# Kernel optimization log

Measured on AMD Instinct MI355X. Metric: run time of the kernel, lower is better.

The kernel has to match this reference:

```python
import jax, jax.numpy as jnp
import numpy as np

N = 50000       # nodes
E = 800000      # edges (avg degree 16)
C_IN = 128
C_OUT = 64
C_HID = 2 * C_OUT  # 128, per Dir_Encoder_GCN


def gcn_conv(x, W, b, src, dst, ew, n):
    """PyG GCNConv: add self-loops (weight 1), symmetric normalization,
    aggregate transformed source features at destination, add bias."""
    loops = jnp.arange(n)
    s = jnp.concatenate([src, loops])                       # [E+N]
    d = jnp.concatenate([dst, loops])                       # [E+N]
    w = jnp.concatenate([ew, jnp.ones((n,), ew.dtype)])     # [E+N]
    deg = jax.ops.segment_sum(w, d, num_segments=n)         # weighted in-degree
    dinv = jnp.where(deg > 0, jax.lax.rsqrt(deg), 0.0)      # deg^{-1/2}
    norm = dinv[s] * w * dinv[d]                            # [E+N]
    xw = x @ W                                              # [n, out]
    out = jax.ops.segment_sum(xw[s] * norm[:, None], d, num_segments=n)
    return out + b


def setup_inputs() -> dict:
    key = jax.random.key(0)
    k1, k2, k3, k4, k5, k6, k7 = jax.random.split(key, 7)
    x = jax.random.normal(k1, (N, C_IN), dtype=jnp.float32)
    edge_index = jax.random.randint(k2, (2, E), 0, N, dtype=jnp.int64)
    edge_weight = jax.random.uniform(k3, (E,), dtype=jnp.float32)
    W1 = jax.random.normal(k4, (C_IN, C_HID), dtype=jnp.float32) * (1.0 / np.sqrt(C_IN))
    b1 = jnp.zeros((C_HID,), dtype=jnp.float32)
    W2 = jax.random.normal(k5, (C_HID, C_OUT), dtype=jnp.float32) * (1.0 / np.sqrt(C_HID))
    b2 = jnp.zeros((C_OUT,), dtype=jnp.float32)
    return {"x": x, "edge_index": edge_index, "edge_weight": edge_weight,
            "W1": W1, "b1": b1, "W2": W2, "b2": b2}


def reference(x, edge_index, edge_weight, W1, b1, W2, b2):
    src, dst = edge_index[0], edge_index[1]
    n = x.shape[0]
    h = jax.nn.elu(gcn_conv(x, W1, b1, src, dst, edge_weight, n))
    return jax.nn.softplus(gcn_conv(h, W2, b2, src, dst, edge_weight, n)) + 1e-4
```

## Files before the change

### kernel.cpp

```cpp
#include <hip/hip_runtime.h>
#include <math.h>

constexpr int CAP    = 48;
constexpr int CAPP   = 49;
constexpr int BIN    = 128;
constexpr int SEGCAP = 2432;
constexpr int CE     = 3136;

typedef short v8s __attribute__((ext_vector_type(8)));
typedef float v4f __attribute__((ext_vector_type(4)));


__device__ __forceinline__ uint f2bf(float f) {
    union { float f; uint i; } v; v.f = f;
    uint r = v.i + 0x7FFFu + ((v.i >> 16) & 1u);
    return r >> 16;
}
__device__ __forceinline__ float bf2f(uint h) {
    union { uint i; float f; } v; v.i = h << 16;
    return v.f;
}
__device__ __forceinline__ void bf8_expand(uint4 q, float* o) {
    uint u[4] = {q.x, q.y, q.z, q.w};
#pragma unroll
    for (int j = 0; j < 4; ++j) {
        union { uint i; float f; } lo, hi;
        lo.i = u[j] << 16;
        hi.i = u[j] & 0xFFFF0000u;
        o[2 * j] = lo.f;
        o[2 * j + 1] = hi.f;
    }
}


__global__ __launch_bounds__(256) void k_p1(const int* __restrict__ src,
                                            const int* __restrict__ dst,
                                            const float* __restrict__ ew,
                                            int* __restrict__ g_bin_cnt,
                                            int2* __restrict__ seg, int E) {
    __shared__ int hist[512];
    __shared__ int base[512];
    const int tid = threadIdx.x;
    const int e0 = blockIdx.x * CE;
    const int e1 = min(e0 + CE, E);

    hist[tid] = 0;
    hist[tid + 256] = 0;
    __syncthreads();
    for (int e = e0 + tid; e < e1; e += 256) atomicAdd(&hist[dst[e] >> 7], 1);
    __syncthreads();
    for (int b = tid; b < 512; b += 256)
        base[b] = (hist[b] > 0) ? atomicAdd(&g_bin_cnt[b], hist[b]) : 0;
    __syncthreads();
    hist[tid] = 0;
    hist[tid + 256] = 0;
    __syncthreads();
    for (int e = e0 + tid; e < e1; e += 256) {
        int d = dst[e];
        int b = d >> 7;
        int r = atomicAdd(&hist[b], 1);
        int slot = base[b] + r;
        if (slot < SEGCAP)
            seg[(size_t)b * SEGCAP + slot] =
                make_int2(((d & 127) << 16) | src[e], __float_as_int(ew[e]));
    }
}


__global__ __launch_bounds__(256) void k_p2(const int* __restrict__ g_bin_cnt,
                                            const int2* __restrict__ seg,
                                            int* __restrict__ cnt, float* __restrict__ dinv,
                                            int2* __restrict__ bucket, int N) {
    __shared__ int2 lb[BIN * CAPP];
    __shared__ int lcnt[BIN];
    __shared__ float ldeg[BIN];
    const int b = blockIdx.x;
    const int tid = threadIdx.x;
    if (tid < BIN) { lcnt[tid] = 0; ldeg[tid] = 0.f; }
    __syncthreads();

    const int m = min(g_bin_cnt[b], SEGCAP);
    const int2* s = seg + (size_t)b * SEGCAP;
    for (int i = tid; i < m; i += 256) {
        int2 p = s[i];
        int dl = (p.x >> 16) & 127;
        int sv = p.x & 0xFFFF;
        int slot = atomicAdd(&lcnt[dl], 1);
        if (slot < CAP) lb[dl * CAPP + slot] = make_int2(sv, p.y);
        atomicAdd(&ldeg[dl], __int_as_float(p.y));
    }
    __syncthreads();

    const int node0 = b * BIN;
    if (tid < BIN && node0 + tid < N) {
        cnt[node0 + tid] = min(lcnt[tid], CAP);
        dinv[node0 + tid] = rsqrtf(1.0f + ldeg[tid]);
    }
    const int nn = min(BIN, N - node0);
    for (int i = tid; i < nn * CAP; i += 256) {
        int nl = i / CAP;
        int j = i - nl * CAP;
        if (j < min(lcnt[nl], CAP))
            bucket[((size_t)node0 + nl) * CAP + j] = lb[nl * CAPP + j];
    }
}


template <int COLS>
__global__ __launch_bounds__(256) void k_pack(const float* __restrict__ W,
                                              ushort* __restrict__ wpk) {
    constexpr int NT = COLS / 16;
    int id = blockIdx.x * 256 + threadIdx.x;
    if (id >= 4 * NT * 64) return;
    int lane = id & 63;
    int t = (id >> 6) % NT;
    int c = (id >> 6) / NT;
    int ncol = t * 16 + (lane & 15);
    int k0 = c * 32 + (lane >> 4) * 8;
    ushort hi[8], lo[8];
#pragma unroll
    for (int j = 0; j < 8; ++j) {
        float v = W[(size_t)(k0 + j) * COLS + ncol];
        ushort h = (ushort)f2bf(v);
        hi[j] = h;
        lo[j] = (ushort)f2bf(v - bf2f(h));
    }
    size_t bh = ((size_t)(c * NT + t) * 64 + lane) * 8;
    size_t bl = ((size_t)((4 + c) * NT + t) * 64 + lane) * 8;
    *(uint4*)(wpk + bh) = *(uint4*)hi;
    *(uint4*)(wpk + bl) = *(uint4*)lo;
}


__global__ __launch_bounds__(256) void k_gemm1(const float* __restrict__ X,
                                               const ushort* __restrict__ wpk,
                                               const float* __restrict__ dinv,
                                               ushort* __restrict__ Y, int n) {
    constexpr int NT = 8;
    const int wave = threadIdx.x >> 6;
    const int lane = threadIdx.x & 63;
    const int m = lane & 15;
    const int q = lane >> 4;
    const int r0 = blockIdx.x * 64 + wave * 16;

    v4f acc[NT];
#pragma unroll
    for (int t = 0; t < NT; ++t) acc[t] = (v4f){0.f, 0.f, 0.f, 0.f};

    const int arow = min(r0 + m, n - 1);

    for (int c = 0; c < 4; ++c) {
        const float* xp = X + (size_t)arow * 128 + c * 32 + q * 8;
        float4 v0 = *(const float4*)xp;
        float4 v1 = *(const float4*)(xp + 4);
        float f[8] = {v0.x, v0.y, v0.z, v0.w, v1.x, v1.y, v1.z, v1.w};
        union { ushort u[8]; v8s v; } H, L;
#pragma unroll
        for (int j = 0; j < 8; ++j) {
            ushort h = (ushort)f2bf(f[j]);
            H.u[j] = h;
            L.u[j] = (ushort)f2bf(f[j] - bf2f(h));
        }
#pragma unroll
        for (int t = 0; t < NT; ++t) {
            v8s b_hi = *(const v8s*)(wpk + ((size_t)(c * NT + t) * 64 + lane) * 8);
            v8s b_lo = *(const v8s*)(wpk + ((size_t)((4 + c) * NT + t) * 64 + lane) * 8);
            acc[t] = __builtin_amdgcn_mfma_f32_16x16x32_bf16(H.v, b_hi, acc[t], 0, 0, 0);
            acc[t] = __builtin_amdgcn_mfma_f32_16x16x32_bf16(H.v, b_lo, acc[t], 0, 0, 0);
            acc[t] = __builtin_amdgcn_mfma_f32_16x16x32_bf16(L.v, b_hi, acc[t], 0, 0, 0);
        }
    }

#pragma unroll
    for (int r = 0; r < 4; ++r) {
        int row = r0 + q * 4 + r;
        if (row < n) {
            float sc = dinv[row];
#pragma unroll
            for (int t = 0; t < NT; ++t)
                Y[(size_t)row * 128 + t * 16 + m] = (ushort)f2bf(acc[t][r] * sc);
        }
    }
}


__global__ __launch_bounds__(256) void k_gather_g2(const ushort* __restrict__ xw,
                                                   const float* __restrict__ dinv,
                                                   const float* __restrict__ b1,
                                                   const int* __restrict__ cnt,
                                                   const int2* __restrict__ bucket,
                                                   const ushort* __restrict__ wpk2,
                                                   ushort* __restrict__ hw, int n) {
    constexpr int HS = 136;
    __shared__ ushort hrow[16 * HS];
    __shared__ float sdd[16];
    const int tid = threadIdx.x;
    const int node_l = tid >> 4;
    const int lane16 = tid & 15;
    const int node0 = blockIdx.x * 16;
    const int node = node0 + node_l;
    const bool active = node < n;

    float acc[8] = {0.f, 0.f, 0.f, 0.f, 0.f, 0.f, 0.f, 0.f};
    if (active) {
        {
            float sf[8];
            uint4 q = *(const uint4*)(xw + (size_t)node * 128 + lane16 * 8);
            bf8_expand(q, sf);
#pragma unroll
            for (int j = 0; j < 8; ++j) acc[j] = sf[j];
        }
        int c = min(cnt[node], CAP);
        const int2* bk = bucket + (size_t)node * CAP;
        int i = 0;
        for (; i + 4 <= c; i += 4) {
            int4 p0 = *(const int4*)(bk + i);
            int4 p1 = *(const int4*)(bk + i + 2);
            float w0 = __int_as_float(p0.y);
            float w1 = __int_as_float(p0.w);
            float w2 = __int_as_float(p1.y);
            float w3 = __int_as_float(p1.w);
            uint4 q0 = *(const uint4*)(xw + (size_t)p0.x * 128 + lane16 * 8);
            uint4 q1 = *(const uint4*)(xw + (size_t)p0.z * 128 + lane16 * 8);
            uint4 q2 = *(const uint4*)(xw + (size_t)p1.x * 128 + lane16 * 8);
            uint4 q3 = *(const uint4*)(xw + (size_t)p1.z * 128 + lane16 * 8);
            float f[8];
            bf8_expand(q0, f);
#pragma unroll
            for (int j = 0; j < 8; ++j) acc[j] += f[j] * w0;
            bf8_expand(q1, f);
#pragma unroll
            for (int j = 0; j < 8; ++j) acc[j] += f[j] * w1;
            bf8_expand(q2, f);
#pragma unroll
            for (int j = 0; j < 8; ++j) acc[j] += f[j] * w2;
            bf8_expand(q3, f);
#pragma unroll
            for (int j = 0; j < 8; ++j) acc[j] += f[j] * w3;
        }
        for (; i < c; ++i) {
            int2 sw = bk[i];
            float w = __int_as_float(sw.y);
            uint4 q = *(const uint4*)(xw + (size_t)sw.x * 128 + lane16 * 8);
            float f[8];
            bf8_expand(q, f);
#pragma unroll
            for (int j = 0; j < 8; ++j) acc[j] += f[j] * w;
        }

        float dd = dinv[node];
        if (lane16 == 0) sdd[node_l] = dd;
        float4 b0 = *(const float4*)(b1 + lane16 * 8);
        float4 bv = *(const float4*)(b1 + lane16 * 8 + 4);
        float bb[8] = {b0.x, b0.y, b0.z, b0.w, bv.x, bv.y, bv.z, bv.w};
#pragma unroll
        for (int j = 0; j < 8; ++j) {
            float v = bb[j] + dd * acc[j];
            acc[j] = v > 0.f ? v : expm1f(v);
        }
    } else {
        if (lane16 == 0) sdd[node_l] = 0.f;
#pragma unroll
        for (int j = 0; j < 8; ++j) acc[j] = 0.f;
    }

    uint4 o;
    o.x = f2bf(acc[0]) | (f2bf(acc[1]) << 16);
    o.y = f2bf(acc[2]) | (f2bf(acc[3]) << 16);
    o.z = f2bf(acc[4]) | (f2bf(acc[5]) << 16);
    o.w = f2bf(acc[6]) | (f2bf(acc[7]) << 16);
    *(uint4*)(hrow + node_l * HS + lane16 * 8) = o;
    __syncthreads();

    const int wave = tid >> 6;
    const int lane = tid & 63;
    const int mm = lane & 15;
    const int qq = lane >> 4;
    v4f c4 = (v4f){0.f, 0.f, 0.f, 0.f};
    for (int c = 0; c < 4; ++c) {
        v8s a = *(const v8s*)(hrow + mm * HS + c * 32 + qq * 8);
        v8s b_hi = *(const v8s*)(wpk2 + ((size_t)(c * 4 + wave) * 64 + lane) * 8);
        v8s b_lo = *(const v8s*)(wpk2 + ((size_t)((4 + c) * 4 + wave) * 64 + lane) * 8);
        c4 = __builtin_amdgcn_mfma_f32_16x16x32_bf16(a, b_hi, c4, 0, 0, 0);
        c4 = __builtin_amdgcn_mfma_f32_16x16x32_bf16(a, b_lo, c4, 0, 0, 0);
    }
#pragma unroll
    for (int r = 0; r < 4; ++r) {
        int nl = qq * 4 + r;
        int row = node0 + nl;
        if (row < n)
            hw[(size_t)row * 64 + wave * 16 + mm] = (ushort)f2bf(c4[r] * sdd[nl]);
    }
}


__global__ __launch_bounds__(256) void k_gather2(const ushort* __restrict__ hw,
                                                 const float* __restrict__ dinv,
                                                 const float* __restrict__ b2,
                                                 const int* __restrict__ cnt,
                                                 const int2* __restrict__ bucket,
                                                 float* __restrict__ out, int n) {
    constexpr int C = 64, L = 8;
    int node = blockIdx.x * 32 + threadIdx.x / L;
    int lane = threadIdx.x % L;
    if (node >= n) return;

    float acc[8];
    {
        float sf[8];
        uint4 q = *(const uint4*)(hw + (size_t)node * C + lane * 8);
        bf8_expand(q, sf);
#pragma unroll
        for (int j = 0; j < 8; ++j) acc[j] = sf[j];
    }

    int c = min(cnt[node], CAP);
    const int2* bk = bucket + (size_t)node * CAP;
    int i = 0;
    for (; i + 4 <= c; i += 4) {
        int4 p0 = *(const int4*)(bk + i);
        int4 p1 = *(const int4*)(bk + i + 2);
        float w0 = __int_as_float(p0.y);
        float w1 = __int_as_float(p0.w);
        float w2 = __int_as_float(p1.y);
        float w3 = __int_as_float(p1.w);
        uint4 q0 = *(const uint4*)(hw + (size_t)p0.x * C + lane * 8);
        uint4 q1 = *(const uint4*)(hw + (size_t)p0.z * C + lane * 8);
        uint4 q2 = *(const uint4*)(hw + (size_t)p1.x * C + lane * 8);
        uint4 q3 = *(const uint4*)(hw + (size_t)p1.z * C + lane * 8);
        float f[8];
        bf8_expand(q0, f);
#pragma unroll
        for (int j = 0; j < 8; ++j) acc[j] += f[j] * w0;
        bf8_expand(q1, f);
#pragma unroll
        for (int j = 0; j < 8; ++j) acc[j] += f[j] * w1;
        bf8_expand(q2, f);
#pragma unroll
        for (int j = 0; j < 8; ++j) acc[j] += f[j] * w2;
        bf8_expand(q3, f);
#pragma unroll
        for (int j = 0; j < 8; ++j) acc[j] += f[j] * w3;
    }
    for (; i < c; ++i) {
        int2 sw = bk[i];
        float w = __int_as_float(sw.y);
        uint4 q = *(const uint4*)(hw + (size_t)sw.x * C + lane * 8);
        float f[8];
        bf8_expand(q, f);
#pragma unroll
        for (int j = 0; j < 8; ++j) acc[j] += f[j] * w;
    }

    float dd = dinv[node];
    float4 b0 = *(const float4*)(b2 + lane * 8);
    float4 bv = *(const float4*)(b2 + lane * 8 + 4);
    float bb[8] = {b0.x, b0.y, b0.z, b0.w, bv.x, bv.y, bv.z, bv.w};
#pragma unroll
    for (int j = 0; j < 8; ++j) {
        float v = bb[j] + dd * acc[j];
        acc[j] = ((v > 20.f) ? v : log1pf(expf(v))) + 1e-4f;
    }
    *(float4*)(out + (size_t)node * C + lane * 8) =
        make_float4(acc[0], acc[1], acc[2], acc[3]);
    *(float4*)(out + (size_t)node * C + lane * 8 + 4) =
        make_float4(acc[4], acc[5], acc[6], acc[7]);
}


extern "C" void kernel_launch(void* const* d_in, const int* in_sizes, int n_in,
                              void* d_out, int out_size, void* d_ws, size_t ws_size,
                              hipStream_t stream) {
    const float* x  = (const float*)d_in[0];
    const int*   ei = (const int*)d_in[1];
    const float* ew = (const float*)d_in[2];
    const float* W1 = (const float*)d_in[3];
    const float* b1 = (const float*)d_in[4];
    const float* W2 = (const float*)d_in[5];
    const float* b2 = (const float*)d_in[6];

    const int N = in_sizes[0] / 128;
    const int E = in_sizes[1] / 2;
    const int* src = ei;
    const int* dst = ei + E;
    float* y = (float*)d_out;

    const int nbins = (N + BIN - 1) / BIN;

    char* p = (char*)d_ws;
    auto take = [&](size_t bytes) {
        char* q = p;
        p += (bytes + 255) & ~(size_t)255;
        return q;
    };

    int*    g_bin_cnt = (int*)take(512 * 4);
    int2*   seg       = (int2*)take((size_t)nbins * SEGCAP * 8);
    int*    cnt       = (int*)take((size_t)N * 4);
    float*  dinv      = (float*)take((size_t)N * 4);
    int2*   bucket    = (int2*)take((size_t)N * CAP * 8);
    ushort* xw        = (ushort*)take((size_t)N * 128 * 2);
    ushort* hw        = (ushort*)take((size_t)N * 64 * 2);
    ushort* wpk1      = (ushort*)take(2 * 4 * 8 * 64 * 8 * 2);
    ushort* wpk2      = (ushort*)take(2 * 4 * 4 * 64 * 8 * 2);

    auto cdiv = [](int a, int b) { return (a + b - 1) / b; };

    hipMemsetAsync(g_bin_cnt, 0, 512 * 4, stream);
    k_p1<<<cdiv(E, CE), 256, 0, stream>>>(src, dst, ew, g_bin_cnt, seg, E);
    k_pack<128><<<8, 256, 0, stream>>>(W1, wpk1);
    k_pack<64><<<4, 256, 0, stream>>>(W2, wpk2);
    k_p2<<<nbins, 256, 0, stream>>>(g_bin_cnt, seg, cnt, dinv, bucket, N);

    k_gemm1<<<cdiv(N, 64), 256, 0, stream>>>(x, wpk1, dinv, xw, N);
    k_gather_g2<<<cdiv(N, 16), 256, 0, stream>>>(xw, dinv, b1, cnt, bucket, wpk2, hw, N);
    k_gather2<<<cdiv(N, 32), 256, 0, stream>>>(hw, dinv, b2, cnt, bucket, y, N);
}
```

Before: 195.5 us.

## Pack bucket entries to 32-bit with bf16 weights, merge prep launches, unroll gathers by 8

Each bucket entry is shrunk from an int2 (source index plus fp32 weight) to a single uint holding a 16-bit source index and a bf16 edge weight. This halves bucket traffic in p2 and in both gather kernels. The memset and the two weight-pack launches are merged into one prep kernel to cut launch overhead. A shared gather helper unrolls by 8 to keep more row loads in flight, at the cost of some edge-weight precision from the bf16 rounding.

```diff
diff --git a/kernel.cpp b/kernel.cpp
--- a/kernel.cpp
+++ b/kernel.cpp
@@ -30,6 +30,47 @@
         o[2 * j] = lo.f;
         o[2 * j + 1] = hi.f;
     }
+}
+
+
+template <int COLS>
+__device__ __forceinline__ void pack_one(const float* __restrict__ W,
+                                         ushort* __restrict__ wpk, int id) {
+    constexpr int NT = COLS / 16;
+    int lane = id & 63;
+    int t = (id >> 6) % NT;
+    int c = (id >> 6) / NT;
+    int ncol = t * 16 + (lane & 15);
+    int k0 = c * 32 + (lane >> 4) * 8;
+    ushort hi[8], lo[8];
+#pragma unroll
+    for (int j = 0; j < 8; ++j) {
+        float v = W[(size_t)(k0 + j) * COLS + ncol];
+        ushort h = (ushort)f2bf(v);
+        hi[j] = h;
+        lo[j] = (ushort)f2bf(v - bf2f(h));
+    }
+    size_t bh = ((size_t)(c * NT + t) * 64 + lane) * 8;
+    size_t bl = ((size_t)((4 + c) * NT + t) * 64 + lane) * 8;
+    *(uint4*)(wpk + bh) = *(uint4*)hi;
+    *(uint4*)(wpk + bl) = *(uint4*)lo;
+}
+
+__global__ __launch_bounds__(256) void k_prep(const float* __restrict__ W1,
+                                              const float* __restrict__ W2,
+                                              ushort* __restrict__ wpk1,
+                                              ushort* __restrict__ wpk2,
+                                              int* __restrict__ g_bin_cnt) {
+    const int blk = blockIdx.x;
+    const int tid = threadIdx.x;
+    if (blk == 0) {
+        g_bin_cnt[tid] = 0;
+        g_bin_cnt[tid + 256] = 0;
+        return;
+    }
+    int id = (blk - 1) * 256 + tid;
+    if (id < 2048) pack_one<128>(W1, wpk1, id);
+    else if (id < 3072) pack_one<64>(W2, wpk2, id - 2048);
 }
 
 
@@ -70,8 +111,8 @@
 __global__ __launch_bounds__(256) void k_p2(const int* __restrict__ g_bin_cnt,
                                             const int2* __restrict__ seg,
                                             int* __restrict__ cnt, float* __restrict__ dinv,
-                                            int2* __restrict__ bucket, int N) {
-    __shared__ int2 lb[BIN * CAPP];
+                                            uint* __restrict__ bucket, int N) {
+    __shared__ uint lb[BIN * CAPP];
     __shared__ int lcnt[BIN];
     __shared__ float ldeg[BIN];
     const int b = blockIdx.x;
@@ -84,10 +125,11 @@
     for (int i = tid; i < m; i += 256) {
         int2 p = s[i];
         int dl = (p.x >> 16) & 127;
-        int sv = p.x & 0xFFFF;
+        uint sv = (uint)(p.x & 0xFFFF);
+        float w = __int_as_float(p.y);
         int slot = atomicAdd(&lcnt[dl], 1);
-        if (slot < CAP) lb[dl * CAPP + slot] = make_int2(sv, p.y);
-        atomicAdd(&ldeg[dl], __int_as_float(p.y));
+        if (slot < CAP) lb[dl * CAPP + slot] = sv | (f2bf(w) << 16);
+        atomicAdd(&ldeg[dl], w);
     }
     __syncthreads();
 
@@ -103,32 +145,6 @@
         if (j < min(lcnt[nl], CAP))
             bucket[((size_t)node0 + nl) * CAP + j] = lb[nl * CAPP + j];
     }
-}
-
-
-template <int COLS>
-__global__ __launch_bounds__(256) void k_pack(const float* __restrict__ W,
-                                              ushort* __restrict__ wpk) {
-    constexpr int NT = COLS / 16;
-    int id = blockIdx.x * 256 + threadIdx.x;
-    if (id >= 4 * NT * 64) return;
-    int lane = id & 63;
-    int t = (id >> 6) % NT;
-    int c = (id >> 6) / NT;
-    int ncol = t * 16 + (lane & 15);
-    int k0 = c * 32 + (lane >> 4) * 8;
-    ushort hi[8], lo[8];
-#pragma unroll
-    for (int j = 0; j < 8; ++j) {
-        float v = W[(size_t)(k0 + j) * COLS + ncol];
-        ushort h = (ushort)f2bf(v);
-        hi[j] = h;
-        lo[j] = (ushort)f2bf(v - bf2f(h));
-    }
-    size_t bh = ((size_t)(c * NT + t) * 64 + lane) * 8;
-    size_t bl = ((size_t)((4 + c) * NT + t) * 64 + lane) * 8;
-    *(uint4*)(wpk + bh) = *(uint4*)hi;
-    *(uint4*)(wpk + bl) = *(uint4*)lo;
 }
 
 
@@ -184,11 +200,61 @@
 }
 
 
+template <int C>
+__device__ __forceinline__ void gather_accum(const ushort* __restrict__ xw,
+                                             const uint* __restrict__ bk, int c,
+                                             int laneoff, float* acc) {
+    int i = 0;
+    for (; i + 8 <= c; i += 8) {
+        uint4 e0 = *(const uint4*)(bk + i);
+        uint4 e1 = *(const uint4*)(bk + i + 4);
+        uint ee[8] = {e0.x, e0.y, e0.z, e0.w, e1.x, e1.y, e1.z, e1.w};
+        uint4 q[8];
+#pragma unroll
+        for (int u = 0; u < 8; ++u)
+            q[u] = *(const uint4*)(xw + (size_t)(ee[u] & 0xFFFF) * C + laneoff);
+#pragma unroll
+        for (int u = 0; u < 8; ++u) {
+            float w = bf2f(ee[u] >> 16);
+            float f[8];
+            bf8_expand(q[u], f);
+#pragma unroll
+            for (int j = 0; j < 8; ++j) acc[j] += f[j] * w;
+        }
+    }
+    for (; i + 4 <= c; i += 4) {
+        uint4 e0 = *(const uint4*)(bk + i);
+        uint ee[4] = {e0.x, e0.y, e0.z, e0.w};
+        uint4 q[4];
+#pragma unroll
+        for (int u = 0; u < 4; ++u)
+            q[u] = *(const uint4*)(xw + (size_t)(ee[u] & 0xFFFF) * C + laneoff);
+#pragma unroll
+        for (int u = 0; u < 4; ++u) {
+            float w = bf2f(ee[u] >> 16);
+            float f[8];
+            bf8_expand(q[u], f);
+#pragma unroll
+            for (int j = 0; j < 8; ++j) acc[j] += f[j] * w;
+        }
+    }
+    for (; i < c; ++i) {
+        uint e = bk[i];
+        float w = bf2f(e >> 16);
+        uint4 qq = *(const uint4*)(xw + (size_t)(e & 0xFFFF) * C + laneoff);
+        float f[8];
+        bf8_expand(qq, f);
+#pragma unroll
+        for (int j = 0; j < 8; ++j) acc[j] += f[j] * w;
+    }
+}
+
+
 __global__ __launch_bounds__(256) void k_gather_g2(const ushort* __restrict__ xw,
                                                    const float* __restrict__ dinv,
                                                    const float* __restrict__ b1,
                                                    const int* __restrict__ cnt,
-                                                   const int2* __restrict__ bucket,
+                                                   const uint* __restrict__ bucket,
                                                    const ushort* __restrict__ wpk2,
                                                    ushort* __restrict__ hw, int n) {
     constexpr int HS = 136;
@@ -211,42 +277,7 @@
             for (int j = 0; j < 8; ++j) acc[j] = sf[j];
         }
         int c = min(cnt[node], CAP);
-        const int2* bk = bucket + (size_t)node * CAP;
-        int i = 0;
-        for (; i + 4 <= c; i += 4) {
-            int4 p0 = *(const int4*)(bk + i);
-            int4 p1 = *(const int4*)(bk + i + 2);
-            float w0 = __int_as_float(p0.y);
-            float w1 = __int_as_float(p0.w);
-            float w2 = __int_as_float(p1.y);
-            float w3 = __int_as_float(p1.w);
-            uint4 q0 = *(const uint4*)(xw + (size_t)p0.x * 128 + lane16 * 8);
-            uint4 q1 = *(const uint4*)(xw + (size_t)p0.z * 128 + lane16 * 8);
-            uint4 q2 = *(const uint4*)(xw + (size_t)p1.x * 128 + lane16 * 8);
-            uint4 q3 = *(const uint4*)(xw + (size_t)p1.z * 128 + lane16 * 8);
-            float f[8];
-            bf8_expand(q0, f);
-#pragma unroll
-            for (int j = 0; j < 8; ++j) acc[j] += f[j] * w0;
-            bf8_expand(q1, f);
-#pragma unroll
-            for (int j = 0; j < 8; ++j) acc[j] += f[j] * w1;
-            bf8_expand(q2, f);
-#pragma unroll
-            for (int j = 0; j < 8; ++j) acc[j] += f[j] * w2;
-            bf8_expand(q3, f);
-#pragma unroll
-            for (int j = 0; j < 8; ++j) acc[j] += f[j] * w3;
-        }
-        for (; i < c; ++i) {
-            int2 sw = bk[i];
-            float w = __int_as_float(sw.y);
-            uint4 q = *(const uint4*)(xw + (size_t)sw.x * 128 + lane16 * 8);
-            float f[8];
-            bf8_expand(q, f);
-#pragma unroll
-            for (int j = 0; j < 8; ++j) acc[j] += f[j] * w;
-        }
+        gather_accum<128>(xw, bucket + (size_t)node * CAP, c, lane16 * 8, acc);
 
         float dd = dinv[node];
         if (lane16 == 0) sdd[node_l] = dd;
@@ -298,7 +329,7 @@
                                                  const float* __restrict__ dinv,
                                                  const float* __restrict__ b2,
                                                  const int* __restrict__ cnt,
-                                                 const int2* __restrict__ bucket,
+                                                 const uint* __restrict__ bucket,
                                                  float* __restrict__ out, int n) {
     constexpr int C = 64, L = 8;
     int node = blockIdx.x * 32 + threadIdx.x / L;
@@ -315,42 +346,7 @@
     }
 
     int c = min(cnt[node], CAP);
-    const int2* bk = bucket + (size_t)node * CAP;
-    int i = 0;
-    for (; i + 4 <= c; i += 4) {
-        int4 p0 = *(const int4*)(bk + i);
-        int4 p1 = *(const int4*)(bk + i + 2);
-        float w0 = __int_as_float(p0.y);
-        float w1 = __int_as_float(p0.w);
-        float w2 = __int_as_float(p1.y);
-        float w3 = __int_as_float(p1.w);
-        uint4 q0 = *(const uint4*)(hw + (size_t)p0.x * C + lane * 8);
-        uint4 q1 = *(const uint4*)(hw + (size_t)p0.z * C + lane * 8);
-        uint4 q2 = *(const uint4*)(hw + (size_t)p1.x * C + lane * 8);
-        uint4 q3 = *(const uint4*)(hw + (size_t)p1.z * C + lane * 8);
-        float f[8];
-        bf8_expand(q0, f);
-#pragma unroll
-        for (int j = 0; j < 8; ++j) acc[j] += f[j] * w0;
-        bf8_expand(q1, f);
-#pragma unroll
-        for (int j = 0; j < 8; ++j) acc[j] += f[j] * w1;
-        bf8_expand(q2, f);
-#pragma unroll
-        for (int j = 0; j < 8; ++j) acc[j] += f[j] * w2;
-        bf8_expand(q3, f);
-#pragma unroll
-        for (int j = 0; j < 8; ++j) acc[j] += f[j] * w3;
-    }
-    for (; i < c; ++i) {
-        int2 sw = bk[i];
-        float w = __int_as_float(sw.y);
-        uint4 q = *(const uint4*)(hw + (size_t)sw.x * C + lane * 8);
-        float f[8];
-        bf8_expand(q, f);
-#pragma unroll
-        for (int j = 0; j < 8; ++j) acc[j] += f[j] * w;
-    }
+    gather_accum<64>(hw, bucket + (size_t)node * CAP, c, lane * 8, acc);
 
     float dd = dinv[node];
     float4 b0 = *(const float4*)(b2 + lane * 8);
@@ -398,7 +394,7 @@
     int2*   seg       = (int2*)take((size_t)nbins * SEGCAP * 8);
     int*    cnt       = (int*)take((size_t)N * 4);
     float*  dinv      = (float*)take((size_t)N * 4);
-    int2*   bucket    = (int2*)take((size_t)N * CAP * 8);
+    uint*   bucket    = (uint*)take((size_t)N * CAP * 4);
     ushort* xw        = (ushort*)take((size_t)N * 128 * 2);
     ushort* hw        = (ushort*)take((size_t)N * 64 * 2);
     ushort* wpk1      = (ushort*)take(2 * 4 * 8 * 64 * 8 * 2);
@@ -406,10 +402,8 @@
 
     auto cdiv = [](int a, int b) { return (a + b - 1) / b; };
 
-    hipMemsetAsync(g_bin_cnt, 0, 512 * 4, stream);
+    k_prep<<<13, 256, 0, stream>>>(W1, W2, wpk1, wpk2, g_bin_cnt);
     k_p1<<<cdiv(E, CE), 256, 0, stream>>>(src, dst, ew, g_bin_cnt, seg, E);
-    k_pack<128><<<8, 256, 0, stream>>>(W1, wpk1);
-    k_pack<64><<<4, 256, 0, stream>>>(W2, wpk2);
     k_p2<<<nbins, 256, 0, stream>>>(g_bin_cnt, seg, cnt, dinv, bucket, N);
 
     k_gemm1<<<cdiv(N, 64), 256, 0, stream>>>(x, wpk1, dinv, xw, N);
```

Result: no change. 192.2 us (-1.7%).
